# Performance work log

Hardware: AMD Instinct MI355X
Metric: run time of the kernel (lower is better)

Reference implementation:

```python
import jax, jax.numpy as jnp
import numpy as np

IN, OUT, S = 4096, 4096, 256
B, T = 4, 2048

# Straight-through-estimator sign quantizer (binary quant of low-rank factors).
@jax.custom_vjp
def ste_sign(x):
    return jnp.sign(x)

def _ste_fwd(x):
    return jnp.sign(x), None

def _ste_bwd(_, g):
    return (g,)

ste_sign.defvjp(_ste_fwd, _ste_bwd)


def setup_inputs() -> dict:
    key = jax.random.key(0)
    ks = jax.random.split(key, 14)
    nrm = lambda k, shp, s: jax.random.normal(k, shp, dtype=jnp.float32) * s
    uni = lambda k, shp: jax.random.uniform(k, shp, dtype=jnp.float32, minval=0.1, maxval=1.0)
    return {
        "x": nrm(ks[0], (B, T, IN), 1.0),
        "V": nrm(ks[1], (S, IN), 0.02),
        "U": nrm(ks[2], (OUT, S), 0.02),
        "v1": uni(ks[3], (1, S)),
        "v2": uni(ks[4], (1, IN)),
        "u1": uni(ks[5], (1, OUT)),
        "u2": uni(ks[6], (1, S)),
        "V_R": nrm(ks[7], (S, IN), 0.02),
        "U_R": nrm(ks[8], (OUT, S), 0.02),
        "v1_R": uni(ks[9], (1, S)),
        "v2_R": uni(ks[10], (1, IN)),
        "u1_R": uni(ks[11], (1, OUT)),
        "u2_R": uni(ks[12], (1, S)),
        "bias": nrm(ks[13], (OUT,), 0.02),
    }


def _branch(x2, V, U, v1, v2, u1, u2):
    # y = (((x * v2) @ sign(V).T) * (v1*u2)) @ sign(U).T * u1   (left-to-right, as in torch)
    Vq = ste_sign(V)          # [S, IN]
    Uq = ste_sign(U)          # [OUT, S]
    h = (x2 * v2) @ Vq.T      # [N, S]
    h = h * (v1 * u2)         # per-rank scale
    y = h @ Uq.T              # [N, OUT]
    return y * u1


def reference(x, V, U, v1, v2, u1, u2, V_R, U_R, v1_R, v2_R, u1_R, u2_R, bias):
    shp = x.shape
    x2 = x.reshape(-1, shp[-1])                                  # [N, IN]
    y = _branch(x2, V, U, v1, v2, u1, u2)
    y = y + _branch(x2, V_R, U_R, v1_R, v2_R, u1_R, u2_R)        # residual low-rank branch
    y = y + bias
    return y.reshape(shp[:-1] + (OUT,))
```

## Files before the change

### kernel.cpp

```cpp
#include <hip/hip_runtime.h>
#include <hip/hip_bf16.h>
#include <stdint.h>
#include <stddef.h>

typedef __attribute__((ext_vector_type(8))) short short8;
typedef __attribute__((ext_vector_type(4))) float floatx4;

#define AS_GLOBAL(p) (const __attribute__((address_space(1))) void*)(p)
#define AS_LDS(p)    (__attribute__((address_space(3))) void*)(p)

static constexpr int IN_DIM  = 4096;
static constexpr int OUT_DIM = 4096;
static constexpr int S_DIM   = 256;
static constexpr int S2      = 512;

__global__ void prep_kernel(const float* __restrict__ V, const float* __restrict__ v2,
                            const float* __restrict__ V_R, const float* __restrict__ v2_R,
                            const float* __restrict__ U, const float* __restrict__ u1,
                            const float* __restrict__ v1, const float* __restrict__ u2,
                            const float* __restrict__ U_R, const float* __restrict__ u1_R,
                            const float* __restrict__ v1_R, const float* __restrict__ u2_R,
                            __hip_bfloat16* __restrict__ W1,
                            __hip_bfloat16* __restrict__ W2) {
  const int bid = blockIdx.x;
  if (bid < 2048) {
    const int idx4 = (bid * 256 + threadIdx.x) * 4;
    const int i = idx4 & (IN_DIM - 1);
    const int s = idx4 >> 12;
    floatx4 w, sc;
    if (s < S_DIM) {
      w  = *(const floatx4*)(V + s * IN_DIM + i);
      sc = *(const floatx4*)(v2 + i);
    } else {
      w  = *(const floatx4*)(V_R + (s - S_DIM) * IN_DIM + i);
      sc = *(const floatx4*)(v2_R + i);
    }
    union { ushort4 v; __hip_bfloat16 h[4]; } u;
#pragma unroll
    for (int j = 0; j < 4; ++j) {
      const float sg = (w[j] > 0.f) ? 1.f : ((w[j] < 0.f) ? -1.f : 0.f);
      u.h[j] = __float2bfloat16(sg * sc[j]);
    }
    *(ushort4*)((unsigned short*)W1 + idx4) = u.v;
  } else {
    const int idx4 = ((bid - 2048) * 256 + threadIdx.x) * 4;
    const int s = idx4 & (S2 - 1);
    const int o = idx4 >> 9;
    floatx4 w, scs;
    float sco;
    if (s < S_DIM) {
      w   = *(const floatx4*)(U + o * S_DIM + s);
      sco = u1[o];
      const floatx4 a = *(const floatx4*)(v1 + s);
      const floatx4 b = *(const floatx4*)(u2 + s);
      scs = a * b;
    } else {
      const int ss = s - S_DIM;
      w   = *(const floatx4*)(U_R + o * S_DIM + ss);
      sco = u1_R[o];
      const floatx4 a = *(const floatx4*)(v1_R + ss);
      const floatx4 b = *(const floatx4*)(u2_R + ss);
      scs = a * b;
    }
    union { ushort4 v; __hip_bfloat16 h[4]; } u;
#pragma unroll
    for (int j = 0; j < 4; ++j) {
      const float sg = (w[j] > 0.f) ? 1.f : ((w[j] < 0.f) ? -1.f : 0.f);
      u.h[j] = __float2bfloat16(sg * sco * scs[j]);
    }
    *(ushort4*)((unsigned short*)W2 + idx4) = u.v;
  }
}

__global__ __launch_bounds__(256, 2)
void gemm1_kernel(const float* __restrict__ X,
                  const __hip_bfloat16* __restrict__ B,
                  __hip_bfloat16* __restrict__ C) {
  constexpr int K = IN_DIM;
  constexpr int N = S2;
  constexpr int BM = 128, BN = 64, BK = 64;

  __shared__ __hip_bfloat16 As[2][BM * BK];
  __shared__ __hip_bfloat16 Bs[2][BN * BK];

  const int t = threadIdx.x;
  const int wave = t >> 6;
  const int lane = t & 63;
  const int r16 = lane & 15;
  const int quad = lane >> 4;

  const int f = blockIdx.x;
  const int c = f & 7;
  const int l = f >> 3;
  const int tm0 = (c * 8 + (l >> 3)) * BM;
  const int tn0 = (l & 7) * BN;

  const int wm = (wave & 1) * 64;
  const int wn = (wave >> 1) * 32;

  floatx4 acc[4][2] = {};

  floatx4 areg[4][2];

  auto loadA = [&](int k0) {
#pragma unroll
    for (int i = 0; i < 4; ++i) {
      const int p = t + i * 256;
      const int row = p >> 3;
      const int ql = (p & 7) ^ (row & 7);
      const float* gp = X + (size_t)(tm0 + row) * K + k0 + ql * 8;
      areg[i][0] = *(const floatx4*)gp;
      areg[i][1] = *(const floatx4*)(gp + 4);
    }
  };
  auto writeA = [&](int buf) {
#pragma unroll
    for (int i = 0; i < 4; ++i) {
      const int p = t + i * 256;
      union { short8 v; __hip_bfloat16 h[8]; } u;
#pragma unroll
      for (int j = 0; j < 4; ++j) u.h[j]     = __float2bfloat16(areg[i][0][j]);
#pragma unroll
      for (int j = 0; j < 4; ++j) u.h[4 + j] = __float2bfloat16(areg[i][1][j]);
      *reinterpret_cast<short8*>((char*)&As[buf][0] + p * 16) = u.v;
    }
  };
  auto stageB = [&](int buf, int k0) {
#pragma unroll
    for (int i = 0; i < 2; ++i) {
      const int p = t + i * 256;
      const int row = p >> 3;
      const int ql = (p & 7) ^ (row & 7);
      const __hip_bfloat16* gp = B + (size_t)(tn0 + row) * K + k0 + ql * 8;
      __builtin_amdgcn_global_load_lds(AS_GLOBAL(gp), AS_LDS((char*)&Bs[buf][0] + p * 16), 16, 0, 0);
    }
  };

  loadA(0);
  stageB(0, 0);
  writeA(0);
  __syncthreads();

  int buf = 0;
  for (int k0 = 0; k0 < K; k0 += BK) {
    const bool next = (k0 + BK < K);
    if (next) { loadA(k0 + BK); stageB(buf ^ 1, k0 + BK); }

    const char* as = (const char*)&As[buf][0];
    const char* bs = (const char*)&Bs[buf][0];
#pragma unroll
    for (int ks = 0; ks < 2; ++ks) {
      short8 a[4], b[2];
      const int cc = ks * 4 + quad;
#pragma unroll
      for (int i = 0; i < 4; ++i) {
        const int ar = wm + i * 16 + r16;
        a[i] = *reinterpret_cast<const short8*>(as + (ar * 8 + (cc ^ (ar & 7))) * 16);
      }
#pragma unroll
      for (int j = 0; j < 2; ++j) {
        const int br = wn + j * 16 + r16;
        b[j] = *reinterpret_cast<const short8*>(bs + (br * 8 + (cc ^ (br & 7))) * 16);
      }
#pragma unroll
      for (int i = 0; i < 4; ++i)
#pragma unroll
        for (int j = 0; j < 2; ++j)
          acc[i][j] = __builtin_amdgcn_mfma_f32_16x16x32_bf16(a[i], b[j], acc[i][j], 0, 0, 0);
    }

    if (next) writeA(buf ^ 1);
    __syncthreads();
    buf ^= 1;
  }

#pragma unroll
  for (int i = 0; i < 4; ++i)
#pragma unroll
    for (int j = 0; j < 2; ++j)
#pragma unroll
      for (int r = 0; r < 4; ++r) {
        const int row = tm0 + wm + i * 16 + quad * 4 + r;
        const int col = tn0 + wn + j * 16 + r16;
        C[(size_t)row * N + col] = __float2bfloat16(acc[i][j][r]);
      }
}

__global__ __launch_bounds__(256, 3)
void gemm2_kernel(const __hip_bfloat16* __restrict__ A,
                  const __hip_bfloat16* __restrict__ B,
                  const float* __restrict__ bias,
                  float* __restrict__ C) {
  constexpr int K = S2;
  constexpr int N = OUT_DIM;
  constexpr int BM = 128, BN = 128, BK = 64;

  __shared__ __hip_bfloat16 As[BM * BK];
  __shared__ __hip_bfloat16 Bs[BN * BK];

  const int t = threadIdx.x;
  const int wave = t >> 6;
  const int lane = t & 63;
  const int r16 = lane & 15;
  const int quad = lane >> 4;

  const int f = blockIdx.x;
  const int c = f & 7;
  const int l = f >> 3;
  const int tm0 = (c * 8 + (l >> 5)) * BM;
  const int tn0 = (l & 31) * BN;

  const int wm = (wave & 1) * 64;
  const int wn = (wave >> 1) * 64;

  floatx4 acc[4][4] = {};

  for (int k0 = 0; k0 < K; k0 += BK) {
#pragma unroll
    for (int i = 0; i < 4; ++i) {
      const int p = t + i * 256;
      const int row = p >> 3;
      const int ql = (p & 7) ^ (row & 7);
      const __hip_bfloat16* gp = A + (size_t)(tm0 + row) * K + k0 + ql * 8;
      __builtin_amdgcn_global_load_lds(AS_GLOBAL(gp), AS_LDS((char*)As + p * 16), 16, 0, 0);
    }
#pragma unroll
    for (int i = 0; i < 4; ++i) {
      const int p = t + i * 256;
      const int row = p >> 3;
      const int ql = (p & 7) ^ (row & 7);
      const __hip_bfloat16* gp = B + (size_t)(tn0 + row) * K + k0 + ql * 8;
      __builtin_amdgcn_global_load_lds(AS_GLOBAL(gp), AS_LDS((char*)Bs + p * 16), 16, 0, 0);
    }
    __syncthreads();

#pragma unroll
    for (int ks = 0; ks < 2; ++ks) {
      short8 a[4], b[4];
      const int cc = ks * 4 + quad;
#pragma unroll
      for (int i = 0; i < 4; ++i) {
        const int ar = wm + i * 16 + r16;
        a[i] = *reinterpret_cast<const short8*>((const char*)As + (ar * 8 + (cc ^ (ar & 7))) * 16);
      }
#pragma unroll
      for (int j = 0; j < 4; ++j) {
        const int br = wn + j * 16 + r16;
        b[j] = *reinterpret_cast<const short8*>((const char*)Bs + (br * 8 + (cc ^ (br & 7))) * 16);
      }
#pragma unroll
      for (int i = 0; i < 4; ++i)
#pragma unroll
        for (int j = 0; j < 4; ++j)
          acc[i][j] = __builtin_amdgcn_mfma_f32_16x16x32_bf16(a[i], b[j], acc[i][j], 0, 0, 0);
    }
    __syncthreads();
  }

  float bi[4];
#pragma unroll
  for (int j = 0; j < 4; ++j) bi[j] = bias[tn0 + wn + j * 16 + r16];

#pragma unroll
  for (int i = 0; i < 4; ++i)
#pragma unroll
    for (int j = 0; j < 4; ++j)
#pragma unroll
      for (int r = 0; r < 4; ++r) {
        const int row = tm0 + wm + i * 16 + quad * 4 + r;
        const int col = tn0 + wn + j * 16 + r16;
        C[(size_t)row * N + col] = acc[i][j][r] + bi[j];
      }
}

extern "C" void kernel_launch(void* const* d_in, const int* in_sizes, int n_in,
                              void* d_out, int out_size, void* d_ws, size_t ws_size,
                              hipStream_t stream) {
  const float* x    = (const float*)d_in[0];
  const float* V    = (const float*)d_in[1];
  const float* U    = (const float*)d_in[2];
  const float* v1   = (const float*)d_in[3];
  const float* v2   = (const float*)d_in[4];
  const float* u1   = (const float*)d_in[5];
  const float* u2   = (const float*)d_in[6];
  const float* V_R  = (const float*)d_in[7];
  const float* U_R  = (const float*)d_in[8];
  const float* v1_R = (const float*)d_in[9];
  const float* v2_R = (const float*)d_in[10];
  const float* u1_R = (const float*)d_in[11];
  const float* u2_R = (const float*)d_in[12];
  const float* bias = (const float*)d_in[13];
  float* out = (float*)d_out;

  const int M = in_sizes[0] / IN_DIM;

  char* ws = (char*)d_ws;
  __hip_bfloat16* W1 = (__hip_bfloat16*)ws;
  __hip_bfloat16* W2 = (__hip_bfloat16*)(ws + (size_t)4 * 1024 * 1024);
  __hip_bfloat16* H  = (__hip_bfloat16*)(ws + (size_t)8 * 1024 * 1024);

  prep_kernel<<<4096, 256, 0, stream>>>(
      V, v2, V_R, v2_R, U, u1, v1, u2, U_R, u1_R, v1_R, u2_R, W1, W2);

  gemm1_kernel<<<(M / 128) * (S2 / 64), 256, 0, stream>>>(x, W1, H);

  gemm2_kernel<<<(M / 128) * (OUT_DIM / 128), 256, 0, stream>>>(H, W2, bias, out);
}
```

Measured before the change: 363.0 us.

## Deepen load pipelining in both GEMMs with explicit vmcnt waits and double buffering

gemm1 now prefetches two K-tiles ahead. It replaces __syncthreads with explicit s_waitcnt vmcnt/lgkmcnt and raw s_barrier, so global loads for tile i+2 stay in flight during compute on tile i. gemm2 gains double-buffered LDS with global_load_lds prefetch of the next tile, and its occupancy hint drops from 3 to 2 blocks per CU. The aim is to hide global memory latency behind MFMA work. The cost is hand-tuned wait counts that must match the instruction counts exactly, plus doubled LDS use in gemm2.

```diff
diff --git a/kernel.cpp b/kernel.cpp
--- a/kernel.cpp
+++ b/kernel.cpp
@@ -8,6 +8,10 @@
 
 #define AS_GLOBAL(p) (const __attribute__((address_space(1))) void*)(p)
 #define AS_LDS(p)    (__attribute__((address_space(3))) void*)(p)
+
+#define WAIT_VM(n)  asm volatile("s_waitcnt vmcnt(" #n ")" ::: "memory")
+#define WAIT_LGKM0() asm volatile("s_waitcnt lgkmcnt(0)" ::: "memory")
+#define SCHED_FENCE() __builtin_amdgcn_sched_barrier(0)
 
 static constexpr int IN_DIM  = 4096;
 static constexpr int OUT_DIM = 4096;
@@ -79,6 +83,7 @@
   constexpr int K = IN_DIM;
   constexpr int N = S2;
   constexpr int BM = 128, BN = 64, BK = 64;
+  constexpr int NT = K / BK;
 
   __shared__ __hip_bfloat16 As[2][BM * BK];
   __shared__ __hip_bfloat16 Bs[2][BN * BK];
@@ -138,14 +143,18 @@
 
   loadA(0);
   stageB(0, 0);
+  WAIT_VM(2); SCHED_FENCE();
   writeA(0);
-  __syncthreads();
-
-  int buf = 0;
-  for (int k0 = 0; k0 < K; k0 += BK) {
-    const bool next = (k0 + BK < K);
-    if (next) { loadA(k0 + BK); stageB(buf ^ 1, k0 + BK); }
-
+  loadA(BK);
+  stageB(1, BK);
+  WAIT_LGKM0(); SCHED_FENCE();
+
+  for (int ti = 0; ti < NT; ++ti) {
+    if (ti < NT - 1) { WAIT_VM(10); } else { WAIT_VM(0); }
+    SCHED_FENCE();
+    __builtin_amdgcn_s_barrier();
+
+    const int buf = ti & 1;
     const char* as = (const char*)&As[buf][0];
     const char* bs = (const char*)&Bs[buf][0];
 #pragma unroll
@@ -169,9 +178,13 @@
           acc[i][j] = __builtin_amdgcn_mfma_f32_16x16x32_bf16(a[i], b[j], acc[i][j], 0, 0, 0);
     }
 
-    if (next) writeA(buf ^ 1);
-    __syncthreads();
-    buf ^= 1;
+    if (ti + 1 < NT) {
+      WAIT_VM(2); SCHED_FENCE();
+      writeA(buf ^ 1);
+      WAIT_LGKM0(); SCHED_FENCE();
+    }
+    __builtin_amdgcn_s_barrier();
+    if (ti + 2 < NT) { loadA((ti + 2) * BK); stageB(buf, (ti + 2) * BK); }
   }
 
 #pragma unroll
@@ -186,7 +199,7 @@
       }
 }
 
-__global__ __launch_bounds__(256, 3)
+__global__ __launch_bounds__(256, 2)
 void gemm2_kernel(const __hip_bfloat16* __restrict__ A,
                   const __hip_bfloat16* __restrict__ B,
                   const float* __restrict__ bias,
@@ -194,9 +207,10 @@
   constexpr int K = S2;
   constexpr int N = OUT_DIM;
   constexpr int BM = 128, BN = 128, BK = 64;
-
-  __shared__ __hip_bfloat16 As[BM * BK];
-  __shared__ __hip_bfloat16 Bs[BN * BK];
+  constexpr int NT = K / BK;
+
+  __shared__ __hip_bfloat16 As[2][BM * BK];
+  __shared__ __hip_bfloat16 Bs[2][BN * BK];
 
   const int t = threadIdx.x;
   const int wave = t >> 6;
@@ -215,14 +229,14 @@
 
   floatx4 acc[4][4] = {};
 
-  for (int k0 = 0; k0 < K; k0 += BK) {
+  auto stage = [&](int buf, int k0) {
 #pragma unroll
     for (int i = 0; i < 4; ++i) {
       const int p = t + i * 256;
       const int row = p >> 3;
       const int ql = (p & 7) ^ (row & 7);
       const __hip_bfloat16* gp = A + (size_t)(tm0 + row) * K + k0 + ql * 8;
-      __builtin_amdgcn_global_load_lds(AS_GLOBAL(gp), AS_LDS((char*)As + p * 16), 16, 0, 0);
+      __builtin_amdgcn_global_load_lds(AS_GLOBAL(gp), AS_LDS((char*)&As[buf][0] + p * 16), 16, 0, 0);
     }
 #pragma unroll
     for (int i = 0; i < 4; ++i) {
@@ -230,10 +244,21 @@
       const int row = p >> 3;
       const int ql = (p & 7) ^ (row & 7);
       const __hip_bfloat16* gp = B + (size_t)(tn0 + row) * K + k0 + ql * 8;
-      __builtin_amdgcn_global_load_lds(AS_GLOBAL(gp), AS_LDS((char*)Bs + p * 16), 16, 0, 0);
-    }
-    __syncthreads();
-
+      __builtin_amdgcn_global_load_lds(AS_GLOBAL(gp), AS_LDS((char*)&Bs[buf][0] + p * 16), 16, 0, 0);
+    }
+  };
+
+  stage(0, 0);
+  stage(1, BK);
+
+  for (int ti = 0; ti < NT; ++ti) {
+    if (ti < NT - 1) { WAIT_VM(8); } else { WAIT_VM(0); }
+    SCHED_FENCE();
+    __builtin_amdgcn_s_barrier();
+
+    const int buf = ti & 1;
+    const char* as = (const char*)&As[buf][0];
+    const char* bs = (const char*)&Bs[buf][0];
 #pragma unroll
     for (int ks = 0; ks < 2; ++ks) {
       short8 a[4], b[4];
@@ -241,12 +266,12 @@
 #pragma unroll
       for (int i = 0; i < 4; ++i) {
         const int ar = wm + i * 16 + r16;
-        a[i] = *reinterpret_cast<const short8*>((const char*)As + (ar * 8 + (cc ^ (ar & 7))) * 16);
+        a[i] = *reinterpret_cast<const short8*>(as + (ar * 8 + (cc ^ (ar & 7))) * 16);
       }
 #pragma unroll
       for (int j = 0; j < 4; ++j) {
         const int br = wn + j * 16 + r16;
-        b[j] = *reinterpret_cast<const short8*>((const char*)Bs + (br * 8 + (cc ^ (br & 7))) * 16);
+        b[j] = *reinterpret_cast<const short8*>(bs + (br * 8 + (cc ^ (br & 7))) * 16);
       }
 #pragma unroll
       for (int i = 0; i < 4; ++i)
@@ -254,7 +279,9 @@
         for (int j = 0; j < 4; ++j)
           acc[i][j] = __builtin_amdgcn_mfma_f32_16x16x32_bf16(a[i], b[j], acc[i][j], 0, 0, 0);
     }
-    __syncthreads();
+
+    __builtin_amdgcn_s_barrier();
+    if (ti + 2 < NT) stage(buf, (ti + 2) * BK);
   }
 
   float bi[4];
```

Result: no change. 366.7 us (+1.0%).
